# Kernel optimization log

Hardware: AMD Instinct MI355X
Metric: run time of the kernel (lower is better)

## Reference

```python
import jax, jax.numpy as jnp
import numpy as np

DIM = 1024
NUM_HEADS = 16
HEAD_DIM = DIM // NUM_HEADS
SCALE = HEAD_DIM ** -0.5


def setup_inputs() -> dict:
    key = jax.random.key(0)
    ks = jax.random.split(key, 6)
    B, N, C = 2, 2048, DIM
    std = C ** -0.5
    return {
        "x_t": jax.random.normal(ks[0], (B, N, C), dtype=jnp.float32),
        "x_s": jax.random.normal(ks[1], (B, N, C), dtype=jnp.float32),
        "W_q": jax.random.normal(ks[2], (C, C), dtype=jnp.float32) * std,
        "W_kv": jax.random.normal(ks[3], (C, 2 * C), dtype=jnp.float32) * std,
        "W_fuse": jax.random.normal(ks[4], (C, C), dtype=jnp.float32) * std,
        "b_fuse": jax.random.normal(ks[5], (C,), dtype=jnp.float32) * 0.01,
    }


def reference(x_t, x_s, W_q, W_kv, W_fuse, b_fuse):
    B, N, C = x_t.shape
    H, D = NUM_HEADS, HEAD_DIM
    # q projection (no bias, qkv_bias=False): [B,N,C] -> [B,H,N,D]
    q = (x_t @ W_q).reshape(B, N, H, D).transpose(0, 2, 1, 3)
    # kv projection: [B,N,2C] -> k,v each [B,H,N,D]
    kv = (x_s @ W_kv).reshape(B, N, 2, H, D).transpose(2, 0, 3, 1, 4)
    k, v = kv[0], kv[1]
    # attention scores [B,H,N,N]
    attn = jnp.einsum("bhnd,bhmd->bhnm", q, k) * SCALE
    attn = jax.nn.softmax(attn, axis=-1)
    # weighted values -> [B,N,C]
    a = jnp.einsum("bhnm,bhmd->bhnd", attn, v).transpose(0, 2, 1, 3).reshape(B, N, C)
    # fuse projection (with bias); dropouts are identity (p=0)
    return a @ W_fuse + b_fuse
```

## Files before the change

kernel.cpp:

```cpp
#include <hip/hip_runtime.h>

#define SEQ 2048

typedef short short8 __attribute__((ext_vector_type(8)));
typedef float floatx4 __attribute__((ext_vector_type(4)));
typedef unsigned int uint2v __attribute__((ext_vector_type(2)));
typedef unsigned int uint4v __attribute__((ext_vector_type(4)));
typedef __fp16 f16x8 __attribute__((ext_vector_type(8)));

static __device__ __forceinline__ unsigned short f2bf(float f) {
    unsigned int u = __builtin_bit_cast(unsigned int, f);
    u = (u + 0x7fffu + ((u >> 16) & 1u)) >> 16;
    return (unsigned short)u;
}

#if __has_builtin(__builtin_amdgcn_cvt_pk_bf16_f32)
typedef __bf16 bf16x2 __attribute__((ext_vector_type(2)));
static __device__ __forceinline__ unsigned int pk_bf16(float a, float b) {
    bf16x2 v = __builtin_amdgcn_cvt_pk_bf16_f32(a, b);
    return __builtin_bit_cast(unsigned int, v);
}
#else
static __device__ __forceinline__ unsigned int pk_bf16(float a, float b) {
    return (unsigned int)f2bf(a) | ((unsigned int)f2bf(b) << 16);
}
#endif

static __device__ __forceinline__ unsigned int pk_f16(float a, float b) {
    auto v = __builtin_amdgcn_cvt_pkrtz(a, b);
    return __builtin_bit_cast(unsigned int, v);
}

#define GLD16(gp, lp)                                                        \
    __builtin_amdgcn_global_load_lds(                                        \
        (const __attribute__((address_space(1))) unsigned int*)(gp),         \
        (__attribute__((address_space(3))) unsigned int*)(lp), 16, 0, 0)

__global__ void prep_kernel(const float4* __restrict__ xa, const float4* __restrict__ xb,
                            ushort4* __restrict__ oa, ushort4* __restrict__ ob, float sa,
                            const float* __restrict__ Wq, const float* __restrict__ Wkv,
                            const float* __restrict__ Wf,
                            unsigned short* __restrict__ oq, unsigned short* __restrict__ okv,
                            unsigned short* __restrict__ of_) {
    __shared__ float tile[32][33];
    int bx = blockIdx.x, tid = threadIdx.x;
    if (bx < 8192) {
        int i = bx * 256 + tid;
        if (i < 1048576) {
            float4 v = xa[i];
            ushort4 o;
            o.x = f2bf(v.x * sa); o.y = f2bf(v.y * sa);
            o.z = f2bf(v.z * sa); o.w = f2bf(v.w * sa);
            oa[i] = o;
        } else {
            int j = i - 1048576;
            float4 v = xb[j];
            ushort4 o;
            o.x = f2bf(v.x); o.y = f2bf(v.y);
            o.z = f2bf(v.z); o.w = f2bf(v.w);
            ob[j] = o;
        }
        return;
    }
    int t2 = bx - 8192;
    const float* in; unsigned short* out; int N, t;
    if (t2 < 1024)      { in = Wq;  out = oq;  N = 1024; t = t2; }
    else if (t2 < 3072) { in = Wkv; out = okv; N = 2048; t = t2 - 1024; }
    else                { in = Wf;  out = of_; N = 1024; t = t2 - 3072; }
    int nb = N >> 5;
    int n0 = (t % nb) * 32, k0 = (t / nb) * 32;
    int tx = tid & 31, ty = tid >> 5;
#pragma unroll
    for (int i = 0; i < 4; i++)
        tile[ty + i * 8][tx] = in[(size_t)(k0 + ty + i * 8) * N + n0 + tx];
    __syncthreads();
#pragma unroll
    for (int i = 0; i < 4; i++)
        out[(size_t)(n0 + ty + i * 8) * 1024 + k0 + tx] = f2bf(tile[tx][ty + i * 8]);
}

__global__ __launch_bounds__(256, 3)
void gemm_qkv(const unsigned short* __restrict__ xt,
              const unsigned short* __restrict__ xs,
              const unsigned short* __restrict__ wq,
              const unsigned short* __restrict__ wkv,
              unsigned short* __restrict__ q_ws,
              unsigned short* __restrict__ k_ws,
              unsigned short* __restrict__ vt_ws) {
    __shared__ __align__(16) unsigned short smem_[16384];
    auto sA = (unsigned short(*)[64])smem_;
    auto sB = (unsigned short(*)[64])(smem_ + 8192);
    int tid = threadIdx.x, wave = tid >> 6, lane = tid & 63;
    int l15 = lane & 15, quad = lane >> 4;
    int cx = blockIdx.x;
    bool isq = cx < 8, isv = cx >= 16;
    const unsigned short* A  = isq ? xt : xs;
    const unsigned short* Bt = isq ? wq : wkv;
    int C0 = (isq ? cx : cx - 8) * 128;
    int R0 = blockIdx.y * 128;
    int wr = (wave >> 1) * 64, wc = (wave & 1) * 64;
    int srow = lane >> 3, scol = (lane & 7) * 8;

    floatx4 acc[4][4];
#pragma unroll
    for (int i = 0; i < 4; i++)
#pragma unroll
        for (int j = 0; j < 4; j++) acc[i][j] = (floatx4){0.f, 0.f, 0.f, 0.f};

    for (int kt = 0; kt < 16; kt++) {
        __syncthreads();
#pragma unroll
        for (int c = 0; c < 4; c++) {
            int rb = wave * 32 + c * 8;
            GLD16(&A [(size_t)(R0 + rb + srow) * 1024 + kt * 64 + scol], &sA[rb][0]);
            GLD16(&Bt[(size_t)(C0 + rb + srow) * 1024 + kt * 64 + scol], &sB[rb][0]);
        }
        __syncthreads();
#pragma unroll
        for (int ks = 0; ks < 2; ks++) {
            short8 af[4], bf[4];
#pragma unroll
            for (int mt = 0; mt < 4; mt++)
                af[mt] = *(const short8*)&sA[wr + mt * 16 + l15][ks * 32 + quad * 8];
#pragma unroll
            for (int nt = 0; nt < 4; nt++)
                bf[nt] = *(const short8*)&sB[wc + nt * 16 + l15][ks * 32 + quad * 8];
#pragma unroll
            for (int mt = 0; mt < 4; mt++)
#pragma unroll
                for (int nt = 0; nt < 4; nt++)
                    acc[mt][nt] = __builtin_amdgcn_mfma_f32_16x16x32_bf16(af[mt], bf[nt], acc[mt][nt], 0, 0, 0);
        }
    }

    int b = R0 >> 11, n0 = R0 & 2047;
    __syncthreads();

    if (!isv) {
#pragma unroll
        for (int mt = 0; mt < 4; mt++)
#pragma unroll
            for (int nt = 0; nt < 4; nt++) {
                int col = wc + nt * 16 + l15;
#pragma unroll
                for (int r = 0; r < 4; r++)
                    smem_[(wr + mt * 16 + quad * 4 + r) * 128 + col] = f2bf(acc[mt][nt][r]);
            }
        __syncthreads();
        unsigned short* out = isq ? q_ws : k_ws;
#pragma unroll
        for (int i = 0; i < 8; i++) {
            int u = tid + i * 256;
            int row = u >> 4, colg = u & 15;
            int n = n0 + row;
            int gc = C0 + colg * 8;
            int h = gc >> 6, d0 = gc & 63;
            int dd = isq ? d0 : ((((d0 >> 3) ^ (n & 7)) << 3));
            *(uint4v*)&out[((size_t)((b * 16 + h) * 2048 + n)) * 64 + dd] =
                *(const uint4v*)&smem_[row * 128 + colg * 8];
        }
    } else {
#pragma unroll
        for (int mt = 0; mt < 4; mt++)
#pragma unroll
            for (int nt = 0; nt < 4; nt++) {
                int cc = wc + nt * 16 + l15;
                int nl4 = (wr + mt * 16 + quad * 4) >> 2;
                int sw = nl4 ^ ((cc & 3) << 1);
                uint2v pk;
                pk.x = pk_f16(acc[mt][nt][0], acc[mt][nt][1]);
                pk.y = pk_f16(acc[mt][nt][2], acc[mt][nt][3]);
                *(uint2v*)&smem_[cc * 128 + (sw << 2)] = pk;
            }
        __syncthreads();
        int cb = C0 - 1024;
#pragma unroll
        for (int i = 0; i < 8; i++) {
            int u = tid + i * 256;
            int cc = u >> 4, ng = u & 15;
            int sw0 = (2 * ng) ^ ((cc & 3) << 1);
            uint4v val = *(const uint4v*)&smem_[cc * 128 + (sw0 << 2)];
            int ccv = cb + cc, h = ccv >> 6, d = ccv & 63;
            *(uint4v*)&vt_ws[((size_t)((b * 16 + h) * 64 + d)) * 2048 + n0 + ng * 8] = val;
        }
    }
}

__global__ __launch_bounds__(256, 3)
void gemm_fuse(const unsigned short* __restrict__ A,
               const unsigned short* __restrict__ Bt,
               float* __restrict__ out, const float* __restrict__ bias) {
    __shared__ unsigned short sA[128][64];
    __shared__ unsigned short sB[64][64];
    int tid = threadIdx.x, wave = tid >> 6, lane = tid & 63;
    int l15 = lane & 15, quad = lane >> 4;
    int R0 = blockIdx.y * 128, C0 = blockIdx.x * 64;
    int wr = (wave >> 1) * 64, wc = (wave & 1) * 32;
    int srow = lane >> 3, scol = (lane & 7) * 8;

    floatx4 acc[4][2];
#pragma unroll
    for (int i = 0; i < 4; i++)
#pragma unroll
        for (int j = 0; j < 2; j++) acc[i][j] = (floatx4){0.f, 0.f, 0.f, 0.f};

    for (int kt = 0; kt < 16; kt++) {
        __syncthreads();
#pragma unroll
        for (int c = 0; c < 4; c++) {
            int rb = wave * 32 + c * 8;
            GLD16(&A[(size_t)(R0 + rb + srow) * 1024 + kt * 64 + scol], &sA[rb][0]);
        }
#pragma unroll
        for (int c = 0; c < 2; c++) {
            int rb = wave * 16 + c * 8;
            GLD16(&Bt[(size_t)(C0 + rb + srow) * 1024 + kt * 64 + scol], &sB[rb][0]);
        }
        __syncthreads();
#pragma unroll
        for (int ks = 0; ks < 2; ks++) {
            short8 af[4], bf[2];
#pragma unroll
            for (int mt = 0; mt < 4; mt++)
                af[mt] = *(const short8*)&sA[wr + mt * 16 + l15][ks * 32 + quad * 8];
#pragma unroll
            for (int nt = 0; nt < 2; nt++)
                bf[nt] = *(const short8*)&sB[wc + nt * 16 + l15][ks * 32 + quad * 8];
#pragma unroll
            for (int mt = 0; mt < 4; mt++)
#pragma unroll
                for (int nt = 0; nt < 2; nt++)
                    acc[mt][nt] = __builtin_amdgcn_mfma_f32_16x16x32_bf16(af[mt], bf[nt], acc[mt][nt], 0, 0, 0);
        }
    }

#pragma unroll
    for (int mt = 0; mt < 4; mt++) {
#pragma unroll
        for (int r = 0; r < 4; r++) {
            int row = R0 + wr + mt * 16 + quad * 4 + r;
#pragma unroll
            for (int nt = 0; nt < 2; nt++) {
                int col = C0 + wc + nt * 16 + l15;
                out[(size_t)row * 1024 + col] = acc[mt][nt][r] + bias[col];
            }
        }
    }
}

__global__ __launch_bounds__(256, 3)
void attn_kernel(const unsigned short* __restrict__ Q,
                 const unsigned short* __restrict__ K,
                 const unsigned short* __restrict__ Vt,
                 unsigned short* __restrict__ Aout) {
    __shared__ __align__(16) unsigned short smem[16384];
    __shared__ float lred[4][4][16];

    int tid = threadIdx.x, wave = tid >> 6, lane = tid & 63;
    int l15 = lane & 15, quad = lane >> 4;

    int id = blockIdx.x;
    int logical = (id & 7) * 128 + (id >> 3);
    int bh = logical >> 5, qt = logical & 31;
    int b = bh >> 4, h = bh & 15;
    int qr0 = qt * 64;

    const unsigned short* Qp = Q + (size_t)bh * SEQ * 64;
    const unsigned short* Kp = K + (size_t)bh * SEQ * 64;
    const unsigned short* Vp = Vt + (size_t)bh * 64 * SEQ;

    int wk0 = wave * 16;
    int WB = wave * 4096;

#define STAGEK(t)                                                             \
    {                                                                         \
        _Pragma("unroll")                                                     \
        for (int j = 0; j < 2; j++)                                           \
            GLD16(&Kp[(size_t)((t) * 64 + wk0 + j * 8 + (lane >> 3)) * 64 +   \
                      (lane & 7) * 8],                                        \
                  &smem[WB + ((t) & 3) * 1024 + j * 512]);                    \
    }

    STAGEK(0) STAGEK(1) STAGEK(2) STAGEK(3)

    short8 qf[4][2];
#pragma unroll
    for (int nt = 0; nt < 4; nt++)
#pragma unroll
        for (int ks = 0; ks < 2; ks++)
            qf[nt][ks] = *(const short8*)&Qp[(size_t)(qr0 + nt * 16 + l15) * 64 + ks * 32 + quad * 8];

    floatx4 of[4][4];
#pragma unroll
    for (int i = 0; i < 4; i++)
#pragma unroll
        for (int j = 0; j < 4; j++) of[i][j] = (floatx4){0.f, 0.f, 0.f, 0.f};
    floatx4 of_l[4];
#pragma unroll
    for (int i = 0; i < 4; i++) of_l[i] = (floatx4){0.f, 0.f, 0.f, 0.f};

    f16x8 vones;
#pragma unroll
    for (int i = 0; i < 8; i++) vones[i] = (__fp16)1.0f;

    int ksw = (l15 & 7) << 3;
    int ka0 = l15 * 64 + ((quad * 8) ^ ksw);
    int ka1 = l15 * 64 + ((32 + quad * 8) ^ ksw);

    auto compute_pair = [&](int p) {
        int b0 = WB + ((2 * p) & 3) * 1024, b1 = b0 + 1024;
        int t0 = 2 * p * 64, t1 = t0 + 64;
        uint2v va[4], vb[4];
#pragma unroll
        for (int dt = 0; dt < 4; dt++) {
            const unsigned short* vr = &Vp[(size_t)(dt * 16 + l15) * 2048 + wk0 + quad * 4];
            va[dt] = *(const uint2v*)&vr[t0];
            vb[dt] = *(const uint2v*)&vr[t1];
        }
        __builtin_amdgcn_s_setprio(1);
        uint2v pka[4], pkb[4];
        {
            short8 kf0 = *(const short8*)&smem[b0 + ka0];
            short8 kf1 = *(const short8*)&smem[b0 + ka1];
#pragma unroll
            for (int nt = 0; nt < 4; nt++) {
                floatx4 z = (floatx4){0.f, 0.f, 0.f, 0.f};
                floatx4 s = __builtin_amdgcn_mfma_f32_16x16x32_bf16(kf0, qf[nt][0], z, 0, 0, 0);
                s = __builtin_amdgcn_mfma_f32_16x16x32_bf16(kf1, qf[nt][1], s, 0, 0, 0);
                pka[nt].x = pk_f16(__builtin_amdgcn_exp2f(s[0]), __builtin_amdgcn_exp2f(s[1]));
                pka[nt].y = pk_f16(__builtin_amdgcn_exp2f(s[2]), __builtin_amdgcn_exp2f(s[3]));
            }
        }
        {
            short8 kf0 = *(const short8*)&smem[b1 + ka0];
            short8 kf1 = *(const short8*)&smem[b1 + ka1];
#pragma unroll
            for (int nt = 0; nt < 4; nt++) {
                floatx4 z = (floatx4){0.f, 0.f, 0.f, 0.f};
                floatx4 s = __builtin_amdgcn_mfma_f32_16x16x32_bf16(kf0, qf[nt][0], z, 0, 0, 0);
                s = __builtin_amdgcn_mfma_f32_16x16x32_bf16(kf1, qf[nt][1], s, 0, 0, 0);
                pkb[nt].x = pk_f16(__builtin_amdgcn_exp2f(s[0]), __builtin_amdgcn_exp2f(s[1]));
                pkb[nt].y = pk_f16(__builtin_amdgcn_exp2f(s[2]), __builtin_amdgcn_exp2f(s[3]));
            }
        }
#pragma unroll
        for (int dt = 0; dt < 4; dt++) {
            f16x8 vf = __builtin_bit_cast(f16x8,
                (uint4v){va[dt].x, va[dt].y, vb[dt].x, vb[dt].y});
#pragma unroll
            for (int nt = 0; nt < 4; nt++) {
                f16x8 pf = __builtin_bit_cast(f16x8,
                    (uint4v){pka[nt].x, pka[nt].y, pkb[nt].x, pkb[nt].y});
                of[dt][nt] = __builtin_amdgcn_mfma_f32_16x16x32_f16(vf, pf, of[dt][nt], 0, 0, 0);
            }
        }
#pragma unroll
        for (int nt = 0; nt < 4; nt++) {
            f16x8 pf = __builtin_bit_cast(f16x8,
                (uint4v){pka[nt].x, pka[nt].y, pkb[nt].x, pkb[nt].y});
            of_l[nt] = __builtin_amdgcn_mfma_f32_16x16x32_f16(vones, pf, of_l[nt], 0, 0, 0);
        }
        __builtin_amdgcn_s_setprio(0);
    };

    asm volatile("s_waitcnt vmcnt(12)" ::: "memory");
    compute_pair(0);
    __builtin_amdgcn_sched_barrier(0);
    STAGEK(4) STAGEK(5)
    __builtin_amdgcn_sched_barrier(0);
    asm volatile("s_waitcnt vmcnt(12)" ::: "memory");
    compute_pair(1);
    __builtin_amdgcn_sched_barrier(0);
    STAGEK(6) STAGEK(7)
    __builtin_amdgcn_sched_barrier(0);
    for (int p = 2; p < 14; p++) {
        asm volatile("s_waitcnt vmcnt(4)" ::: "memory");
        compute_pair(p);
        __builtin_amdgcn_sched_barrier(0);
        STAGEK(2 * p + 4) STAGEK(2 * p + 5)
        __builtin_amdgcn_sched_barrier(0);
    }
    asm volatile("s_waitcnt vmcnt(4)" ::: "memory");
    compute_pair(14);
    asm volatile("s_waitcnt vmcnt(0)" ::: "memory");
    compute_pair(15);
#undef STAGEK

    if (quad == 0) {
#pragma unroll
        for (int nt = 0; nt < 4; nt++) lred[wave][nt][l15] = of_l[nt][0];
    }
    __syncthreads();

    float* red = (float*)smem;

#define RED_WRITE(C, DTC)                                                          \
    _Pragma("unroll")                                                              \
    for (int nt = 0; nt < 4; nt++)                                                 \
        *(floatx4*)&red[((C) * 4 + wave) * 1024 + nt * 256 + lane * 4] = of[DTC][nt];

#define RED_STORE(DT, C, W0, W1, W2)                                               \
    {                                                                              \
        size_t obase = (size_t)(b * SEQ + qr0) * 1024 + h * 64 + (DT) * 16 + quad * 4; \
        _Pragma("unroll")                                                          \
        for (int nt = 0; nt < 4; nt++) {                                           \
            floatx4 a0 = *(const floatx4*)&red[((C) * 4 + (W0)) * 1024 + nt * 256 + lane * 4]; \
            floatx4 a1 = *(const floatx4*)&red[((C) * 4 + (W1)) * 1024 + nt * 256 + lane * 4]; \
            floatx4 a2 = *(const floatx4*)&red[((C) * 4 + (W2)) * 1024 + nt * 256 + lane * 4]; \
            floatx4 s = of[DT][nt] + a0 + a1 + a2;                                 \
            float lt = lred[0][nt][l15] + lred[1][nt][l15] + lred[2][nt][l15] + lred[3][nt][l15]; \
            float inv = 1.f / lt;                                                  \
            uint2v o;                                                              \
            o.x = pk_bf16(s[0] * inv, s[1] * inv);                                 \
            o.y = pk_bf16(s[2] * inv, s[3] * inv);                                 \
            *(uint2v*)&Aout[obase + (size_t)(nt * 16 + l15) * 1024] = o;           \
        }                                                                          \
    }

    RED_WRITE(0, 0)
    RED_WRITE(1, 1)
    __syncthreads();
    if (wave == 0)      RED_STORE(0, 0, 1, 2, 3)
    else if (wave == 1) RED_STORE(1, 1, 0, 2, 3)
    __syncthreads();
    RED_WRITE(0, 2)
    RED_WRITE(1, 3)
    __syncthreads();
    if (wave == 2)      RED_STORE(2, 0, 0, 1, 3)
    else if (wave == 3) RED_STORE(3, 1, 0, 1, 2)
#undef RED_WRITE
#undef RED_STORE
}

extern "C" void kernel_launch(void* const* d_in, const int* in_sizes, int n_in,
                              void* d_out, int out_size, void* d_ws, size_t ws_size,
                              hipStream_t stream) {
    const float* x_t  = (const float*)d_in[0];
    const float* x_s  = (const float*)d_in[1];
    const float* W_q  = (const float*)d_in[2];
    const float* W_kv = (const float*)d_in[3];
    const float* W_f  = (const float*)d_in[4];
    const float* b_f  = (const float*)d_in[5];
    float* out = (float*)d_out;

    char* ws = (char*)d_ws;
    const size_t MB = 1u << 20;
    unsigned short* xt_bf = (unsigned short*)(ws);
    unsigned short* xs_bf = (unsigned short*)(ws + 8 * MB);
    unsigned short* wq_t  = (unsigned short*)(ws + 16 * MB);
    unsigned short* wkv_t = (unsigned short*)(ws + 18 * MB);
    unsigned short* wf_t  = (unsigned short*)(ws + 22 * MB);
    unsigned short* q_ws  = (unsigned short*)(ws + 24 * MB);
    unsigned short* k_ws  = (unsigned short*)(ws + 32 * MB);
    unsigned short* vt_ws = (unsigned short*)(ws + 40 * MB);
    unsigned short* a_ws  = (unsigned short*)(ws + 48 * MB);

    prep_kernel<<<12288, 256, 0, stream>>>((const float4*)x_t, (const float4*)x_s,
                                           (ushort4*)xt_bf, (ushort4*)xs_bf,
                                           0.125f * 1.44269504088896340736f,
                                           W_q, W_kv, W_f, wq_t, wkv_t, wf_t);

    gemm_qkv<<<dim3(24, 32), 256, 0, stream>>>(xt_bf, xs_bf, wq_t, wkv_t, q_ws, k_ws, vt_ws);
    attn_kernel<<<1024, 256, 0, stream>>>(q_ws, k_ws, vt_ws, a_ws);
    gemm_fuse<<<dim3(16, 32), 256, 0, stream>>>(a_ws, wf_t, out, b_f);
}
```

Baseline: 232.6 us.

## Stage V tiles through LDS with shared double-buffered K/V pipeline

The attention kernel now stages V alongside K into LDS using direct global-to-LDS 16-byte loads with an XOR swizzle. Previously each lane read V fragments straight from global memory in small 8-byte strided loads. The K/V ring becomes a double buffer of two 64-key tile pairs shared by all waves, so workgroup barriers are now needed around each stage. LDS use doubles and the launch bound drops from 3 to 2 blocks per CU. The aim is coalesced V traffic and less global latency inside the compute loop, at the cost of occupancy and extra barrier synchronisation.

```diff
diff --git a/kernel.cpp b/kernel.cpp
--- a/kernel.cpp
+++ b/kernel.cpp
@@ -248,12 +248,12 @@
     }
 }
 
-__global__ __launch_bounds__(256, 3)
+__global__ __launch_bounds__(256, 2)
 void attn_kernel(const unsigned short* __restrict__ Q,
                  const unsigned short* __restrict__ K,
                  const unsigned short* __restrict__ Vt,
                  unsigned short* __restrict__ Aout) {
-    __shared__ __align__(16) unsigned short smem[16384];
+    __shared__ __align__(16) unsigned short smem[32768];
     __shared__ float lred[4][4][16];
 
     int tid = threadIdx.x, wave = tid >> 6, lane = tid & 63;
@@ -269,19 +269,21 @@
     const unsigned short* Kp = K + (size_t)bh * SEQ * 64;
     const unsigned short* Vp = Vt + (size_t)bh * 64 * SEQ;
 
+    int srow = lane >> 3, scol = (lane & 7) * 8;
     int wk0 = wave * 16;
-    int WB = wave * 4096;
-
-#define STAGEK(t)                                                             \
+    int vscol = scol ^ (srow << 3);
+
+#define STAGE(t, kb)                                                          \
     {                                                                         \
         _Pragma("unroll")                                                     \
-        for (int j = 0; j < 2; j++)                                           \
-            GLD16(&Kp[(size_t)((t) * 64 + wk0 + j * 8 + (lane >> 3)) * 64 +   \
-                      (lane & 7) * 8],                                        \
-                  &smem[WB + ((t) & 3) * 1024 + j * 512]);                    \
-    }
-
-    STAGEK(0) STAGEK(1) STAGEK(2) STAGEK(3)
+        for (int j = 0; j < 2; j++) {                                         \
+            int rb = wk0 + j * 8;                                             \
+            GLD16(&Kp[(size_t)((t) * 64 + rb + srow) * 64 + scol],            \
+                  &smem[(kb) + rb * 64]);                                     \
+            GLD16(&Vp[(size_t)(rb + srow) * 2048 + (t) * 64 + vscol],         \
+                  &smem[16384 + (kb) + rb * 64]);                             \
+        }                                                                     \
+    }
 
     short8 qf[4][2];
 #pragma unroll
@@ -290,6 +292,8 @@
         for (int ks = 0; ks < 2; ks++)
             qf[nt][ks] = *(const short8*)&Qp[(size_t)(qr0 + nt * 16 + l15) * 64 + ks * 32 + quad * 8];
 
+    STAGE(0, 0) STAGE(1, 4096) STAGE(2, 8192) STAGE(3, 12288)
+
     floatx4 of[4][4];
 #pragma unroll
     for (int i = 0; i < 4; i++)
@@ -303,25 +307,21 @@
 #pragma unroll
     for (int i = 0; i < 8; i++) vones[i] = (__fp16)1.0f;
 
+    int krow = wk0 + l15;
     int ksw = (l15 & 7) << 3;
-    int ka0 = l15 * 64 + ((quad * 8) ^ ksw);
-    int ka1 = l15 * 64 + ((32 + quad * 8) ^ ksw);
-
-    auto compute_pair = [&](int p) {
-        int b0 = WB + ((2 * p) & 3) * 1024, b1 = b0 + 1024;
-        int t0 = 2 * p * 64, t1 = t0 + 64;
-        uint2v va[4], vb[4];
-#pragma unroll
-        for (int dt = 0; dt < 4; dt++) {
-            const unsigned short* vr = &Vp[(size_t)(dt * 16 + l15) * 2048 + wk0 + quad * 4];
-            va[dt] = *(const uint2v*)&vr[t0];
-            vb[dt] = *(const uint2v*)&vr[t1];
-        }
+    int kaddr0 = krow * 64 + ((quad * 8) ^ ksw);
+    int kaddr1 = krow * 64 + ((32 + quad * 8) ^ ksw);
+    int vcol = (wk0 + quad * 4) ^ ksw;
+
+    asm volatile("s_waitcnt vmcnt(0)" ::: "memory");
+    __syncthreads();
+
+    auto compute_pair = [&](int kb) {
         __builtin_amdgcn_s_setprio(1);
         uint2v pka[4], pkb[4];
         {
-            short8 kf0 = *(const short8*)&smem[b0 + ka0];
-            short8 kf1 = *(const short8*)&smem[b0 + ka1];
+            short8 kf0 = *(const short8*)&smem[kb + kaddr0];
+            short8 kf1 = *(const short8*)&smem[kb + kaddr1];
 #pragma unroll
             for (int nt = 0; nt < 4; nt++) {
                 floatx4 z = (floatx4){0.f, 0.f, 0.f, 0.f};
@@ -332,8 +332,8 @@
             }
         }
         {
-            short8 kf0 = *(const short8*)&smem[b1 + ka0];
-            short8 kf1 = *(const short8*)&smem[b1 + ka1];
+            short8 kf0 = *(const short8*)&smem[kb + 4096 + kaddr0];
+            short8 kf1 = *(const short8*)&smem[kb + 4096 + kaddr1];
 #pragma unroll
             for (int nt = 0; nt < 4; nt++) {
                 floatx4 z = (floatx4){0.f, 0.f, 0.f, 0.f};
@@ -345,46 +345,41 @@
         }
 #pragma unroll
         for (int dt = 0; dt < 4; dt++) {
-            f16x8 vf = __builtin_bit_cast(f16x8,
-                (uint4v){va[dt].x, va[dt].y, vb[dt].x, vb[dt].y});
+            int vbase = 16384 + kb + (dt * 16 + l15) * 64 + vcol;
+            uint2v va = *(const uint2v*)&smem[vbase];
+            uint2v vb = *(const uint2v*)&smem[vbase + 4096];
+            f16x8 vf = __builtin_bit_cast(f16x8, (uint4v){va.x, va.y, vb.x, vb.y});
 #pragma unroll
             for (int nt = 0; nt < 4; nt++) {
-                f16x8 pf = __builtin_bit_cast(f16x8,
-                    (uint4v){pka[nt].x, pka[nt].y, pkb[nt].x, pkb[nt].y});
+                f16x8 pf = __builtin_bit_cast(f16x8, (uint4v){pka[nt].x, pka[nt].y, pkb[nt].x, pkb[nt].y});
                 of[dt][nt] = __builtin_amdgcn_mfma_f32_16x16x32_f16(vf, pf, of[dt][nt], 0, 0, 0);
             }
         }
 #pragma unroll
         for (int nt = 0; nt < 4; nt++) {
-            f16x8 pf = __builtin_bit_cast(f16x8,
-                (uint4v){pka[nt].x, pka[nt].y, pkb[nt].x, pkb[nt].y});
+            f16x8 pf = __builtin_bit_cast(f16x8, (uint4v){pka[nt].x, pka[nt].y, pkb[nt].x, pkb[nt].y});
             of_l[nt] = __builtin_amdgcn_mfma_f32_16x16x32_f16(vones, pf, of_l[nt], 0, 0, 0);
         }
         __builtin_amdgcn_s_setprio(0);
     };
 
-    asm volatile("s_waitcnt vmcnt(12)" ::: "memory");
+#pragma unroll 2
+    for (int p = 0; p < 14; p++) {
+        int kb = (p & 1) * 8192;
+        compute_pair(kb);
+        __builtin_amdgcn_sched_barrier(0);
+        asm volatile("s_barrier" ::: "memory");
+        STAGE(2 * p + 4, kb)
+        STAGE(2 * p + 5, kb + 4096)
+        asm volatile("s_waitcnt vmcnt(8)" ::: "memory");
+        asm volatile("s_barrier" ::: "memory");
+        __builtin_amdgcn_sched_barrier(0);
+    }
     compute_pair(0);
-    __builtin_amdgcn_sched_barrier(0);
-    STAGEK(4) STAGEK(5)
-    __builtin_amdgcn_sched_barrier(0);
-    asm volatile("s_waitcnt vmcnt(12)" ::: "memory");
-    compute_pair(1);
-    __builtin_amdgcn_sched_barrier(0);
-    STAGEK(6) STAGEK(7)
-    __builtin_amdgcn_sched_barrier(0);
-    for (int p = 2; p < 14; p++) {
-        asm volatile("s_waitcnt vmcnt(4)" ::: "memory");
-        compute_pair(p);
-        __builtin_amdgcn_sched_barrier(0);
-        STAGEK(2 * p + 4) STAGEK(2 * p + 5)
-        __builtin_amdgcn_sched_barrier(0);
-    }
-    asm volatile("s_waitcnt vmcnt(4)" ::: "memory");
-    compute_pair(14);
     asm volatile("s_waitcnt vmcnt(0)" ::: "memory");
-    compute_pair(15);
-#undef STAGEK
+    asm volatile("s_barrier" ::: "memory");
+    compute_pair(8192);
+#undef STAGE
 
     if (quad == 0) {
 #pragma unroll
```

After: 199.5 us. -14.2%, faster.
